# Optimization experiments

Hardware: AMD Instinct MI355X
Metric: run time of the kernel (lower is better)

Reference implementation:

```python
import jax, jax.numpy as jnp
import numpy as np

B, S, H = 1, 2048, 4608
NH, NKV, HD = 36, 4, 128
GROUP = NH // NKV  # 9
ROPE_THETA = 100000.0
SLIDING_WINDOW = 1024


def _rope_tables(seq_len, head_dim):
    inv_freq = 1.0 / (ROPE_THETA ** (jnp.arange(0, head_dim, 2, dtype=jnp.float32) / head_dim))
    ang = jnp.arange(seq_len, dtype=jnp.float32)[:, None] * inv_freq[None, :]  # [S, HD/2]
    emb = jnp.concatenate([ang, ang], axis=-1)  # [S, HD]
    return jnp.cos(emb), jnp.sin(emb)


def setup_inputs() -> dict:
    key = jax.random.key(0)
    ks = jax.random.split(key, 10)
    std = 0.02
    cos_table, sin_table = _rope_tables(S, HD)
    return {
        "hidden_states": jax.random.normal(ks[0], (B, S, H), jnp.float32),
        "position_ids": jnp.broadcast_to(jnp.arange(S, dtype=jnp.int64)[None, :], (B, S)),
        "cos_table": cos_table,
        "sin_table": sin_table,
        "q_w": jax.random.normal(ks[1], (NH * HD, H), jnp.float32) * std,
        "q_b": jax.random.normal(ks[2], (NH * HD,), jnp.float32) * std,
        "k_w": jax.random.normal(ks[3], (NKV * HD, H), jnp.float32) * std,
        "k_b": jax.random.normal(ks[4], (NKV * HD,), jnp.float32) * std,
        "v_w": jax.random.normal(ks[5], (NKV * HD, H), jnp.float32) * std,
        "v_b": jax.random.normal(ks[6], (NKV * HD,), jnp.float32) * std,
        "o_w": jax.random.normal(ks[7], (H, NH * HD), jnp.float32) * std,
        "o_b": jax.random.normal(ks[8], (H,), jnp.float32) * std,
        "sliding_window": SLIDING_WINDOW,
    }


def _rotate_half(x):
    x1, x2 = jnp.split(x, 2, axis=-1)
    return jnp.concatenate([-x2, x1], axis=-1)


def reference(hidden_states, position_ids, cos_table, sin_table,
              q_w, q_b, k_w, k_b, v_w, v_b, o_w, o_b, sliding_window):
    bsz, q_len, _ = hidden_states.shape
    scaling = HD ** -0.5

    q = (hidden_states @ q_w.T + q_b).reshape(bsz, q_len, NH, HD)
    k = (hidden_states @ k_w.T + k_b).reshape(bsz, q_len, NKV, HD)
    v = (hidden_states @ v_w.T + v_b).reshape(bsz, q_len, NKV, HD)

    # RoPE with explicit cos/sin, unsqueeze_dim=2 ('bsnd' layout)
    cos = cos_table[position_ids][:, :, None, :]  # [B, S, 1, HD]
    sin = sin_table[position_ids][:, :, None, :]
    q = q * cos + _rotate_half(q) * sin
    k = k * cos + _rotate_half(k) * sin

    # GQA: group Q heads per KV head
    qg = q.reshape(bsz, q_len, NKV, GROUP, HD)
    logits = jnp.einsum('bqgrd,bkgd->bgrqk', qg, k) * scaling  # [B, NKV, GROUP, S, S]

    # causal + sliding-window mask: attend where k <= q and q - k < window
    idx = jnp.arange(q_len)
    mask = (idx[:, None] >= idx[None, :]) & (idx[:, None] - idx[None, :] < sliding_window)
    logits = jnp.where(mask[None, None, None, :, :], logits, jnp.finfo(logits.dtype).min)

    probs = jax.nn.softmax(logits, axis=-1)
    attn = jnp.einsum('bgrqk,bkgd->bqgrd', probs, v).reshape(bsz, q_len, NH * HD)
    return attn @ o_w.T + o_b
```

## Files before the change

kernel.cpp:

```cpp
#include <hip/hip_runtime.h>
#include <stdint.h>

typedef __attribute__((ext_vector_type(8))) __bf16 bf16x8;
typedef __attribute__((ext_vector_type(4))) float f32x4;
typedef __attribute__((ext_vector_type(8))) unsigned short u16x8;
typedef __attribute__((ext_vector_type(4))) unsigned short u16x4;

#define SEQ 2048
#define HID 4608
#define NQKV 5632
#define NHEAD 36
#define NKVH 4
#define HDIM 128
#define WINDOW 1024

__device__ __forceinline__ unsigned short f2b(float f) {
    unsigned u = __builtin_bit_cast(unsigned, f);
    u += 0x7fffu + ((u >> 16) & 1u);
    return (unsigned short)(u >> 16);
}
__device__ __forceinline__ float b2f(unsigned short h) {
    unsigned u = ((unsigned)h) << 16;
    return __builtin_bit_cast(float, u);
}

#define GLD16(gp, lp) __builtin_amdgcn_global_load_lds( \
    (const __attribute__((address_space(1))) void*)(gp), \
    (__attribute__((address_space(3))) void*)(lp), 16, 0, 0)

#define VMCNT8() asm volatile("s_waitcnt vmcnt(8)" ::: "memory")
#define VMCNT4() asm volatile("s_waitcnt vmcnt(4)" ::: "memory")
#define VMCNT0() asm volatile("s_waitcnt vmcnt(0)" ::: "memory")
#define BARRIER() asm volatile("s_barrier" ::: "memory")

__global__ __launch_bounds__(256) void conv_all_kernel(
    const float* __restrict__ s0, unsigned short* __restrict__ d0, int n0,
    const float* __restrict__ s1, unsigned short* __restrict__ d1, int n1,
    const float* __restrict__ s2, unsigned short* __restrict__ d2, int n2,
    const float* __restrict__ s3, unsigned short* __restrict__ d3, int n3)
{
    int total = n0 + n1 + n2 + n3;
    int stride = gridDim.x * blockDim.x;
    for (int i = blockIdx.x * blockDim.x + threadIdx.x; i < total; i += stride) {
        const float* src; unsigned short* dst; int j = i;
        if (j < n0) { src = s0; dst = d0; }
        else if ((j -= n0) < n1) { src = s1; dst = d1; }
        else if ((j -= n1) < n2) { src = s2; dst = d2; }
        else { j -= n2; src = s3; dst = d3; }
        float4 v = ((const float4*)src)[j];
        ushort4 o;
        o.x = f2b(v.x); o.y = f2b(v.y); o.z = f2b(v.z); o.w = f2b(v.w);
        ((ushort4*)dst)[j] = o;
    }
}

__global__ __launch_bounds__(512, 2) void gemm256_kernel(
    const unsigned short* __restrict__ A,
    const unsigned short* __restrict__ W,
    void* __restrict__ out,
    const float* __restrict__ b0, const float* __restrict__ b1, const float* __restrict__ b2,
    int N, int K, int GX, int GB, int outf32,
    const float* __restrict__ cw_src, unsigned short* __restrict__ cw_dst, int cw_n4)
{
    const int tid = threadIdx.x;
    const int o = blockIdx.x;

    if (o >= GB) {
        int cb = o - GB, ncb = gridDim.x - GB;
        int stride = ncb * 512;
        for (int i = cb * 512 + tid; i < cw_n4; i += stride) {
            float4 v = ((const float4*)cw_src)[i];
            ushort4 u;
            u.x = f2b(v.x); u.y = f2b(v.y); u.z = f2b(v.z); u.w = f2b(v.w);
            ((ushort4*)cw_dst)[i] = u;
        }
        return;
    }

    __shared__ alignas(16) unsigned short ldsA[2][256 * 64];
    __shared__ alignas(16) unsigned short ldsB[2][256 * 64];

    const int w = tid >> 6, lane = tid & 63;
    const int r16 = lane & 15, kg = lane >> 4;
    const int wm = w >> 2, wn = w & 3;

    const int cpx = GB >> 3;
    const int id = (o & 7) * cpx + (o >> 3);
    const int bx = id % GX, by = id / GX;
    const int row0 = by * 256, col0 = bx * 256;

    const int lr = lane >> 3;
    const int lc = lane & 7;
    const int cg = lc ^ lr;
    const unsigned short* Abase = A + (size_t)row0 * K;
    const unsigned short* Wbase = W + (size_t)col0 * K;

    auto STG = [&](const unsigned short* Mat, unsigned short* ldsSlot, int hf, int kb) {
#pragma unroll
        for (int j = 0; j < 2; ++j) {
            int row = hf * 128 + (w * 2 + j) * 8 + lr;
            GLD16(Mat + (size_t)row * K + kb + cg * 8,
                  (char*)ldsSlot + hf * 16384 + (w * 2 + j) * 1024);
        }
    };

    const int NITER = K >> 7;
    f32x4 acc[8][4] = {};
    const int swz = r16 & 7;

    bf16x8 af[4][2], bfA[2][2], bfB[2][2];

#define DSR_A(mh, Sl) \
_Pragma("unroll") for (int mi = 0; mi < 4; ++mi) \
_Pragma("unroll") for (int kh = 0; kh < 2; ++kh) \
    af[mi][kh] = *(const bf16x8*)((Sl) + (wm * 128 + (mh) * 64 + mi * 16 + r16) * 64 + ((kh * 4 + kg) ^ swz) * 8);
#define DSR_B(nh, Sl, BF) \
_Pragma("unroll") for (int ni = 0; ni < 2; ++ni) \
_Pragma("unroll") for (int kh = 0; kh < 2; ++kh) \
    BF[ni][kh] = *(const bf16x8*)((Sl) + (wn * 64 + (nh) * 32 + ni * 16 + r16) * 64 + ((kh * 4 + kg) ^ swz) * 8);
#define MFMA_Q(mh, nh, BF) \
    asm volatile("s_waitcnt lgkmcnt(0)" ::: "memory"); \
    __builtin_amdgcn_sched_barrier(0); \
    __builtin_amdgcn_s_setprio(1); \
_Pragma("unroll") for (int mi = 0; mi < 4; ++mi) \
_Pragma("unroll") for (int ni = 0; ni < 2; ++ni) \
_Pragma("unroll") for (int kh = 0; kh < 2; ++kh) \
    acc[(mh) * 4 + mi][(nh) * 2 + ni] = __builtin_amdgcn_mfma_f32_16x16x32_bf16(af[mi][kh], BF[ni][kh], acc[(mh) * 4 + mi][(nh) * 2 + ni], 0, 0, 0); \
    __builtin_amdgcn_s_setprio(0); \
    __builtin_amdgcn_sched_barrier(0);

    STG(Abase, ldsA[0], 0, 0);  STG(Abase, ldsA[0], 1, 0);
    STG(Wbase, ldsB[0], 0, 0);  STG(Wbase, ldsB[0], 1, 0);
    STG(Abase, ldsA[1], 0, 64); STG(Abase, ldsA[1], 1, 64);
    STG(Wbase, ldsB[1], 0, 64); STG(Wbase, ldsB[1], 1, 64);
    VMCNT0();
    BARRIER();

    for (int i = 0; i < NITER; ++i) {
        const unsigned short* A0 = ldsA[0];
        const unsigned short* B0 = ldsB[0];
        const unsigned short* A1 = ldsA[1];
        const unsigned short* B1 = ldsB[1];
        const bool st = (i + 1 < NITER);
        const int kb0 = (i + 1) * 128;
        const int kb1 = kb0 + 64;

        DSR_A(0, A0); DSR_B(0, B0, bfA);
        BARRIER();
        MFMA_Q(0, 0, bfA);
        BARRIER();
        DSR_B(1, B0, bfB);
        BARRIER();
        MFMA_Q(0, 1, bfB);
        BARRIER();
        DSR_A(1, A0);
        if (st) STG(Wbase, ldsB[0], 0, kb0);
        BARRIER();
        MFMA_Q(1, 1, bfB);
        BARRIER();
        if (st) { STG(Abase, ldsA[0], 0, kb0); VMCNT4(); } else { VMCNT0(); }
        BARRIER();
        MFMA_Q(1, 0, bfA);
        BARRIER();
        DSR_A(0, A1); DSR_B(0, B1, bfA);
        if (st) STG(Abase, ldsA[0], 1, kb0);
        BARRIER();
        MFMA_Q(0, 0, bfA);
        BARRIER();
        DSR_B(1, B1, bfB);
        if (st) STG(Wbase, ldsB[0], 1, kb0);
        BARRIER();
        MFMA_Q(0, 1, bfB);
        BARRIER();
        DSR_A(1, A1);
        if (st) { STG(Wbase, ldsB[1], 0, kb1); STG(Wbase, ldsB[1], 1, kb1); }
        BARRIER();
        MFMA_Q(1, 1, bfB);
        BARRIER();
        if (st) { STG(Abase, ldsA[1], 0, kb1); STG(Abase, ldsA[1], 1, kb1); VMCNT8(); }
        BARRIER();
        MFMA_Q(1, 0, bfA);
        BARRIER();
    }

    if (!outf32) {
        unsigned short* O = (unsigned short*)out;
#pragma unroll
        for (int m = 0; m < 8; ++m)
#pragma unroll
            for (int n = 0; n < 4; ++n)
#pragma unroll
                for (int r = 0; r < 4; ++r) {
                    int row = row0 + wm * 128 + m * 16 + kg * 4 + r;
                    int col = col0 + wn * 64 + n * 16 + r16;
                    float bias = (col < HID) ? b0[col]
                               : (col < HID + 512 ? b1[col - HID] : b2[col - HID - 512]);
                    O[(size_t)row * N + col] = f2b(acc[m][n][r] + bias);
                }
    } else {
        float* O = (float*)out;
#pragma unroll
        for (int m = 0; m < 8; ++m)
#pragma unroll
            for (int n = 0; n < 4; ++n)
#pragma unroll
                for (int r = 0; r < 4; ++r) {
                    int row = row0 + wm * 128 + m * 16 + kg * 4 + r;
                    int col = col0 + wn * 64 + n * 16 + r16;
                    O[(size_t)row * N + col] = acc[m][n][r] + b0[col];
                }
    }
#undef DSR_A
#undef DSR_B
#undef MFMA_Q
}

__global__ __launch_bounds__(256) void rope_kernel(unsigned short* __restrict__ qkv,
                                                   const float* __restrict__ cos_t,
                                                   const float* __restrict__ sin_t) {
    int idx = blockIdx.x * 256 + threadIdx.x;
    int d = idx & 63;
    int t = idx >> 6;
    int head = t % 40;
    int s = t / 40;
    int base = head < NHEAD ? head * HDIM : HID + (head - NHEAD) * HDIM;
    size_t off = (size_t)s * NQKV + base;
    float x = b2f(qkv[off + d]);
    float y = b2f(qkv[off + d + 64]);
    float c = cos_t[s * HDIM + d];
    float sn = sin_t[s * HDIM + d];
    qkv[off + d]      = f2b(x * c - y * sn);
    qkv[off + d + 64] = f2b(y * c + x * sn);
}

__global__ __launch_bounds__(256) void vtrans_kernel(const unsigned short* __restrict__ qkv,
                                                     unsigned short* __restrict__ vtg) {
    __shared__ unsigned short tile[32][36];
    const int s0 = blockIdx.x * 32, d0 = blockIdx.y * 32, kvh = blockIdx.z;
    const int lid = threadIdx.x;
    {
        int sl = lid >> 3, dc = (lid & 7) * 4;
        u16x4 v = *(const u16x4*)(qkv + (size_t)(s0 + sl) * NQKV + HID + 512 + kvh * HDIM + d0 + dc);
#pragma unroll
        for (int i = 0; i < 4; ++i) tile[sl][dc + i] = v[i];
    }
    __syncthreads();
    {
        int dl = lid >> 3, sc = (lid & 7) * 4;
        u16x4 v;
#pragma unroll
        for (int i = 0; i < 4; ++i) v[i] = tile[sc + i][dl];
        *(u16x4*)(vtg + (size_t)kvh * HDIM * SEQ + (size_t)(d0 + dl) * SEQ + s0 + sc) = v;
    }
}

#define KSTR 136
#define VSTR 72
#define PSTR 88
__global__ __launch_bounds__(256) void attn_kernel(const unsigned short* __restrict__ qkv,
                                                   const unsigned short* __restrict__ vtg,
                                                   unsigned short* __restrict__ aout)
{
    __shared__ alignas(16) unsigned short Ks[64 * KSTR];
    __shared__ alignas(16) unsigned short Vt[128 * VSTR];
    __shared__ alignas(16) unsigned short Ps[4 * 16 * PSTR];
    const int h = blockIdx.x, qb = blockIdx.y;
    const int q0 = qb * 64;
    const int kvh = h / 9;
    const int tid = threadIdx.x, wid = tid >> 6, lane = tid & 63;
    const int r16 = lane & 15, kg = lane >> 4;
    const int qbase = q0 + wid * 16;
    const unsigned short* vsrc = vtg + (size_t)kvh * HDIM * SEQ;

    bf16x8 qf[4];
    {
        const unsigned short* qrow = qkv + (size_t)(qbase + r16) * NQKV + h * HDIM;
#pragma unroll
        for (int kk = 0; kk < 4; ++kk)
            qf[kk] = *(const bf16x8*)(qrow + kk * 32 + kg * 8);
    }

    f32x4 o[8] = {};
    float mrow[4], lrow[4];
#pragma unroll
    for (int r = 0; r < 4; ++r) { mrow[r] = -1e30f; lrow[r] = 0.f; }

    int lo = q0 - (WINDOW - 1); if (lo < 0) lo = 0; lo &= ~63;
    unsigned short* myP = Ps + wid * 16 * PSTR;
    const float scale = 0.08838834764831845f;

    u16x8 kreg[4], vreg[4];
#define PREF(KT) \
_Pragma("unroll") for (int j = 0; j < 4; ++j) { \
        int c = tid + j * 256; \
        int key = c >> 4, dc = c & 15; \
        kreg[j] = *(const u16x8*)(qkv + (size_t)((KT) + key) * NQKV + HID + kvh * HDIM + dc * 8); \
        int d = c >> 3, k8 = (c & 7) * 8; \
        vreg[j] = *(const u16x8*)(vsrc + (size_t)d * SEQ + (KT) + k8); \
    }

    PREF(lo);

    for (int kt = lo; kt <= q0; kt += 64) {
#pragma unroll
        for (int j = 0; j < 4; ++j) {
            int c = tid + j * 256;
            int key = c >> 4, dc = c & 15;
            *(u16x8*)(Ks + key * KSTR + dc * 8) = kreg[j];
            int d = c >> 3, k8 = (c & 7) * 8;
            *(u16x8*)(Vt + d * VSTR + k8) = vreg[j];
        }
        __syncthreads();

        if (kt + 64 <= q0) { PREF(kt + 64); }

        f32x4 sc[4] = {};
#pragma unroll
        for (int t = 0; t < 4; ++t)
#pragma unroll
            for (int kk = 0; kk < 4; ++kk) {
                bf16x8 kf = *(const bf16x8*)(Ks + (t * 16 + r16) * KSTR + kk * 32 + kg * 8);
                sc[t] = __builtin_amdgcn_mfma_f32_16x16x32_bf16(qf[kk], kf, sc[t], 0, 0, 0);
            }

        float p[4][4], mt[4];
#pragma unroll
        for (int r = 0; r < 4; ++r) mt[r] = -1e30f;
#pragma unroll
        for (int t = 0; t < 4; ++t)
#pragma unroll
            for (int r = 0; r < 4; ++r) {
                int q = qbase + kg * 4 + r;
                int key = kt + t * 16 + r16;
                bool valid = (key <= q) && (q - key < WINDOW);
                float v = valid ? sc[t][r] * scale : -1e30f;
                p[t][r] = v;
                mt[r] = fmaxf(mt[r], v);
            }
#pragma unroll
        for (int mask = 1; mask <= 8; mask <<= 1)
#pragma unroll
            for (int r = 0; r < 4; ++r)
                mt[r] = fmaxf(mt[r], __shfl_xor(mt[r], mask, 64));

        float alpha[4], tsum[4];
#pragma unroll
        for (int r = 0; r < 4; ++r) {
            float mnew = fmaxf(mrow[r], mt[r]);
            alpha[r] = __expf(mrow[r] - mnew);
            mrow[r] = mnew;
            tsum[r] = 0.f;
        }
#pragma unroll
        for (int t = 0; t < 4; ++t)
#pragma unroll
            for (int r = 0; r < 4; ++r) {
                float e = __expf(p[t][r] - mrow[r]);
                p[t][r] = e;
                tsum[r] += e;
            }
#pragma unroll
        for (int mask = 1; mask <= 8; mask <<= 1)
#pragma unroll
            for (int r = 0; r < 4; ++r)
                tsum[r] += __shfl_xor(tsum[r], mask, 64);
#pragma unroll
        for (int r = 0; r < 4; ++r)
            lrow[r] = lrow[r] * alpha[r] + tsum[r];
#pragma unroll
        for (int n = 0; n < 8; ++n)
#pragma unroll
            for (int r = 0; r < 4; ++r)
                o[n][r] = o[n][r] * alpha[r];

#pragma unroll
        for (int t = 0; t < 4; ++t)
#pragma unroll
            for (int r = 0; r < 4; ++r)
                myP[(kg * 4 + r) * PSTR + t * 16 + r16] = f2b(p[t][r]);
        asm volatile("s_waitcnt lgkmcnt(0)" ::: "memory");

#pragma unroll
        for (int kc = 0; kc < 2; ++kc) {
            bf16x8 pa = *(const bf16x8*)(myP + r16 * PSTR + kc * 32 + kg * 8);
#pragma unroll
            for (int n = 0; n < 8; ++n) {
                bf16x8 vb = *(const bf16x8*)(Vt + (n * 16 + r16) * VSTR + kc * 32 + kg * 8);
                o[n] = __builtin_amdgcn_mfma_f32_16x16x32_bf16(pa, vb, o[n], 0, 0, 0);
            }
        }
        BARRIER();
    }
#undef PREF

#pragma unroll
    for (int n = 0; n < 8; ++n)
#pragma unroll
        for (int r = 0; r < 4; ++r) {
            int q = qbase + kg * 4 + r;
            aout[(size_t)q * HID + h * HDIM + n * 16 + r16] = f2b(o[n][r] / lrow[r]);
        }
}

extern "C" void kernel_launch(void* const* d_in, const int* in_sizes, int n_in,
                              void* d_out, int out_size, void* d_ws, size_t ws_size,
                              hipStream_t stream) {
    const float* hidden = (const float*)d_in[0];
    const float* cos_t = (const float*)d_in[2];
    const float* sin_t = (const float*)d_in[3];
    const float* q_w = (const float*)d_in[4];
    const float* q_b = (const float*)d_in[5];
    const float* k_w = (const float*)d_in[6];
    const float* k_b = (const float*)d_in[7];
    const float* v_w = (const float*)d_in[8];
    const float* v_b = (const float*)d_in[9];
    const float* o_w = (const float*)d_in[10];
    const float* o_b = (const float*)d_in[11];

    char* ws = (char*)d_ws;
    unsigned short* hbf  = (unsigned short*)ws;
    unsigned short* attn = hbf;
    unsigned short* wqkv = (unsigned short*)(ws + 18874368);
    unsigned short* vtg  = wqkv;
    unsigned short* wo   = (unsigned short*)(ws + 70778880);
    unsigned short* qkv  = (unsigned short*)(ws + 113246208);

    dim3 blk(256);
    conv_all_kernel<<<4096, blk, 0, stream>>>(
        hidden, hbf,                          (SEQ * HID) / 4,
        q_w,    wqkv,                         (HID * HID) / 4,
        k_w,    wqkv + (size_t)HID * HID,     (512 * HID) / 4,
        v_w,    wqkv + (size_t)5120 * HID,    (512 * HID) / 4);

    gemm256_kernel<<<dim3(256), dim3(512), 0, stream>>>(
        hbf, wqkv, qkv, q_b, k_b, v_b, NQKV, HID, 22, 176, 0,
        o_w, wo, (HID * HID) / 4);
    rope_kernel<<<(SEQ * 40 * 64) / 256, blk, 0, stream>>>(qkv, cos_t, sin_t);
    vtrans_kernel<<<dim3(SEQ / 32, HDIM / 32, NKVH), blk, 0, stream>>>(qkv, vtg);
    attn_kernel<<<dim3(NHEAD, SEQ / 64), blk, 0, stream>>>(qkv, vtg, attn);
    gemm256_kernel<<<dim3(144), dim3(512), 0, stream>>>(
        attn, wo, d_out, o_b, nullptr, nullptr, HID, HID, 18, 144, 1,
        nullptr, nullptr, 0);
}
```

Baseline: 419.7 us.

## Add 256x192-tile GEMM kernel for output projection to fill more CUs

Adds a new gemm192 kernel with 256x192 tiles and uses it for the output projection in place of the 256x256-tile GEMM. The grid grows from 144 to 192 workgroups, which fits the MI355X's 256 CUs better. The kernel has its own double-buffered LDS pipeline with interleaved staging and waitcnts. Smaller N tiles reduce per-block reuse of A and make the new pipeline schedule more complex.

```diff
diff --git a/kernel.cpp b/kernel.cpp
--- a/kernel.cpp
+++ b/kernel.cpp
@@ -29,6 +29,8 @@
     (__attribute__((address_space(3))) void*)(lp), 16, 0, 0)
 
 #define VMCNT8() asm volatile("s_waitcnt vmcnt(8)" ::: "memory")
+#define VMCNT7() asm volatile("s_waitcnt vmcnt(7)" ::: "memory")
+#define VMCNT5() asm volatile("s_waitcnt vmcnt(5)" ::: "memory")
 #define VMCNT4() asm volatile("s_waitcnt vmcnt(4)" ::: "memory")
 #define VMCNT0() asm volatile("s_waitcnt vmcnt(0)" ::: "memory")
 #define BARRIER() asm volatile("s_barrier" ::: "memory")
@@ -215,6 +217,155 @@
 #undef MFMA_Q
 }
 
+__global__ __launch_bounds__(512, 1) void gemm192_kernel(
+    const unsigned short* __restrict__ A,
+    const unsigned short* __restrict__ W,
+    float* __restrict__ out,
+    const float* __restrict__ b0,
+    int N, int K, int GX)
+{
+    __shared__ alignas(16) unsigned short ldsA[2][256 * 64];
+    __shared__ alignas(16) unsigned short ldsB[2][192 * 64];
+
+    const int tid = threadIdx.x;
+    const int w = tid >> 6, lane = tid & 63;
+    const int r16 = lane & 15, kg = lane >> 4;
+    const int wm = w >> 2, wn = w & 3;
+
+    const int cpx = gridDim.x >> 3;
+    const int o = blockIdx.x;
+    const int id = (o & 7) * cpx + (o >> 3);
+    const int bx = id % GX, by = id / GX;
+    const int row0 = by * 256, col0 = bx * 192;
+
+    const int lr = lane >> 3;
+    const int lc = lane & 7;
+    const int cg = lc ^ lr;
+    const unsigned short* Abase = A + (size_t)row0 * K;
+    const unsigned short* Wbase = W + (size_t)col0 * K;
+
+    auto STGA = [&](unsigned short* slot, int hf, int kb) {
+#pragma unroll
+        for (int j = 0; j < 2; ++j) {
+            int row = hf * 128 + (w * 2 + j) * 8 + lr;
+            GLD16(Abase + (size_t)row * K + kb + cg * 8,
+                  (char*)slot + hf * 16384 + (w * 2 + j) * 1024);
+        }
+    };
+    auto STGB = [&](unsigned short* slot, int j3, int kb) {
+        int row = j3 * 64 + w * 8 + lr;
+        GLD16(Wbase + (size_t)row * K + kb + cg * 8,
+              (char*)slot + j3 * 8192 + w * 1024);
+    };
+
+    const int NITER = K >> 7;
+    f32x4 acc[8][3] = {};
+    const int swz = r16 & 7;
+
+    bf16x8 af[4][2], bf2[2][2], bf1[2];
+
+#define DSR_A(mh, Sl) \
+_Pragma("unroll") for (int mi = 0; mi < 4; ++mi) \
+_Pragma("unroll") for (int kh = 0; kh < 2; ++kh) \
+    af[mi][kh] = *(const bf16x8*)((Sl) + (wm * 128 + (mh) * 64 + mi * 16 + r16) * 64 + ((kh * 4 + kg) ^ swz) * 8);
+#define DSR_B2(Sl) \
+_Pragma("unroll") for (int ni = 0; ni < 2; ++ni) \
+_Pragma("unroll") for (int kh = 0; kh < 2; ++kh) \
+    bf2[ni][kh] = *(const bf16x8*)((Sl) + (wn * 48 + ni * 16 + r16) * 64 + ((kh * 4 + kg) ^ swz) * 8);
+#define DSR_B1(Sl) \
+_Pragma("unroll") for (int kh = 0; kh < 2; ++kh) \
+    bf1[kh] = *(const bf16x8*)((Sl) + (wn * 48 + 32 + r16) * 64 + ((kh * 4 + kg) ^ swz) * 8);
+#define MFMA_Q2(mh) \
+    asm volatile("s_waitcnt lgkmcnt(0)" ::: "memory"); \
+    __builtin_amdgcn_sched_barrier(0); \
+    __builtin_amdgcn_s_setprio(1); \
+_Pragma("unroll") for (int mi = 0; mi < 4; ++mi) \
+_Pragma("unroll") for (int ni = 0; ni < 2; ++ni) \
+_Pragma("unroll") for (int kh = 0; kh < 2; ++kh) \
+    acc[(mh) * 4 + mi][ni] = __builtin_amdgcn_mfma_f32_16x16x32_bf16(af[mi][kh], bf2[ni][kh], acc[(mh) * 4 + mi][ni], 0, 0, 0); \
+    __builtin_amdgcn_s_setprio(0); \
+    __builtin_amdgcn_sched_barrier(0);
+#define MFMA_Q1(mh) \
+    asm volatile("s_waitcnt lgkmcnt(0)" ::: "memory"); \
+    __builtin_amdgcn_sched_barrier(0); \
+    __builtin_amdgcn_s_setprio(1); \
+_Pragma("unroll") for (int mi = 0; mi < 4; ++mi) \
+_Pragma("unroll") for (int kh = 0; kh < 2; ++kh) \
+    acc[(mh) * 4 + mi][2] = __builtin_amdgcn_mfma_f32_16x16x32_bf16(af[mi][kh], bf1[kh], acc[(mh) * 4 + mi][2], 0, 0, 0); \
+    __builtin_amdgcn_s_setprio(0); \
+    __builtin_amdgcn_sched_barrier(0);
+
+    STGA(ldsA[0], 0, 0);  STGA(ldsA[0], 1, 0);
+    STGB(ldsB[0], 0, 0);  STGB(ldsB[0], 1, 0);  STGB(ldsB[0], 2, 0);
+    STGA(ldsA[1], 0, 64); STGA(ldsA[1], 1, 64);
+    STGB(ldsB[1], 0, 64); STGB(ldsB[1], 1, 64); STGB(ldsB[1], 2, 64);
+    VMCNT0();
+    BARRIER();
+
+    for (int i = 0; i < NITER; ++i) {
+        const unsigned short* A0 = ldsA[0];
+        const unsigned short* B0 = ldsB[0];
+        const unsigned short* A1 = ldsA[1];
+        const unsigned short* B1 = ldsB[1];
+        const bool st = (i + 1 < NITER);
+        const int kb0 = (i + 1) * 128;
+        const int kb1 = kb0 + 64;
+
+        DSR_A(0, A0); DSR_B2(B0);
+        BARRIER();
+        MFMA_Q2(0);
+        BARRIER();
+        DSR_B1(B0);
+        BARRIER();
+        MFMA_Q1(0);
+        BARRIER();
+        DSR_A(1, A0);
+        if (st) { STGB(ldsB[0], 0, kb0); STGB(ldsB[0], 1, kb0); STGB(ldsB[0], 2, kb0); }
+        BARRIER();
+        MFMA_Q1(1);
+        BARRIER();
+        if (st) { STGA(ldsA[0], 0, kb0); VMCNT5(); } else { VMCNT0(); }
+        BARRIER();
+        MFMA_Q2(1);
+        BARRIER();
+        DSR_A(0, A1); DSR_B2(B1);
+        if (st) STGA(ldsA[0], 1, kb0);
+        BARRIER();
+        MFMA_Q2(0);
+        BARRIER();
+        DSR_B1(B1);
+        BARRIER();
+        MFMA_Q1(0);
+        BARRIER();
+        DSR_A(1, A1);
+        if (st) { STGB(ldsB[1], 0, kb1); STGB(ldsB[1], 1, kb1); STGB(ldsB[1], 2, kb1);
+                  STGA(ldsA[1], 0, kb1); }
+        BARRIER();
+        MFMA_Q1(1);
+        BARRIER();
+        if (st) { STGA(ldsA[1], 1, kb1); VMCNT7(); }
+        BARRIER();
+        MFMA_Q2(1);
+        BARRIER();
+    }
+
+#pragma unroll
+    for (int m = 0; m < 8; ++m)
+#pragma unroll
+        for (int n = 0; n < 3; ++n)
+#pragma unroll
+            for (int r = 0; r < 4; ++r) {
+                int row = row0 + wm * 128 + m * 16 + kg * 4 + r;
+                int col = col0 + wn * 48 + n * 16 + r16;
+                out[(size_t)row * N + col] = acc[m][n][r] + b0[col];
+            }
+#undef DSR_A
+#undef DSR_B2
+#undef DSR_B1
+#undef MFMA_Q2
+#undef MFMA_Q1
+}
+
 __global__ __launch_bounds__(256) void rope_kernel(unsigned short* __restrict__ qkv,
                                                    const float* __restrict__ cos_t,
                                                    const float* __restrict__ sin_t) {
@@ -438,7 +589,6 @@
     rope_kernel<<<(SEQ * 40 * 64) / 256, blk, 0, stream>>>(qkv, cos_t, sin_t);
     vtrans_kernel<<<dim3(SEQ / 32, HDIM / 32, NKVH), blk, 0, stream>>>(qkv, vtg);
     attn_kernel<<<dim3(NHEAD, SEQ / 64), blk, 0, stream>>>(qkv, vtg, attn);
-    gemm256_kernel<<<dim3(144), dim3(512), 0, stream>>>(
-        attn, wo, d_out, o_b, nullptr, nullptr, HID, HID, 18, 144, 1,
-        nullptr, nullptr, 0);
-}
+    gemm192_kernel<<<dim3(192), dim3(512), 0, stream>>>(
+        attn, wo, (float*)d_out, o_b, HID, HID, 24);
+}
```

Result: faster. 407.5 us (-2.9%).
